# Performance work log

Hardware: AMD Instinct MI355X
Metric: run time of the kernel (lower is better)

The kernel has to match this reference:

```python
import jax, jax.numpy as jnp
import numpy as np

I, H, B, T = 17, 128, 32768, 19

def setup_inputs() -> dict:
    key = jax.random.key(0)
    ks = jax.random.split(key, 7)
    s = 1.0 / np.sqrt(H)  # PyTorch LSTMCell/Linear init scale
    u = lambda k, shape: jax.random.uniform(k, shape, jnp.float32, -s, s)
    return {
        "x": jax.random.normal(ks[0], (B, T, I), jnp.float32),
        "W_ih": u(ks[1], (4 * H, I)),
        "W_hh": u(ks[2], (4 * H, H)),
        "b_ih": u(ks[3], (4 * H,)),
        "b_hh": u(ks[4], (4 * H,)),
        "W_out": u(ks[5], (I, H)),
        "b_out": u(ks[6], (I,)),
    }

def reference(x, W_ih, W_hh, b_ih, b_hh, W_out, b_out):
    B_, T_, _ = x.shape
    Hh = W_hh.shape[1]
    # Precompute input projections for all timesteps in one GEMM: [B,T,4H]
    x_proj = jnp.einsum('bti,gi->btg', x, W_ih) + b_ih + b_hh

    def step(carry, xp_t):
        h, c = carry
        gates = xp_t + h @ W_hh.T            # [B,4H]
        i_g, f_g, g_g, o_g = jnp.split(gates, 4, axis=-1)
        c = jax.nn.sigmoid(f_g) * c + jax.nn.sigmoid(i_g) * jnp.tanh(g_g)
        h = jax.nn.sigmoid(o_g) * jnp.tanh(c)
        y = h @ W_out.T + b_out              # [B,I]
        return (h, c), y

    h0 = jnp.zeros((B_, Hh), x.dtype)
    c0 = jnp.zeros((B_, Hh), x.dtype)
    _, ys = jax.lax.scan(step, (h0, c0), jnp.swapaxes(x_proj, 0, 1))  # ys: [T,B,I]
    return jnp.swapaxes(ys, 0, 1)  # [B,T,I]
```

## Files before the change

kernel.cpp:

```cpp
#include <hip/hip_runtime.h>

#define I_DIM 17
#define H_DIM 128
#define T_DIM 19
#define B_DIM 32768
#define M_ROWS 128
#define NTHR 512
#define GRID (B_DIM / M_ROWS)
#define XI 323
#define NF (M_ROWS * XI)
#define XSLOT 4352

#define OFF_H 0
#define OFF_X 65536
#define OFF_WO 148224
#define LDS_TOT 156416

typedef __bf16 bf16x8 __attribute__((ext_vector_type(8)));
typedef float f32x4 __attribute__((ext_vector_type(4)));
union FragU { bf16x8 v; unsigned short s[8]; uint4 u; };

#define K1 1.4426950408889634f
#define K2 2.8853900817779268f

__device__ __forceinline__ unsigned short f2bf(float f) {
    union { float f; unsigned u; } x; x.f = f;
    return (unsigned short)((x.u + 0x8000u) >> 16);
}

#define SYNC_LDS() do {                                        \
    asm volatile("s_waitcnt lgkmcnt(0)" ::: "memory");         \
    __builtin_amdgcn_s_barrier();                              \
} while (0)

#define MFMA_Q(P_, QT_, ACC_, REC_) do {                                          \
    _Pragma("unroll") for (int m2 = 0; m2 < 2; ++m2) {                            \
        _Pragma("unroll") for (int g = 0; g < 4; ++g)                             \
            ACC_[m2][g] = (f32x4){bias[g], bias[g], bias[g], bias[g]};            \
        FragU fx; fx.u = (uint4){0u, 0u, 0u, 0u};                                 \
        if (q < 2)                                                                \
            fx.v = *(const bf16x8*)(smem + xyA + ((QT_) * 2 + m2) * 512);         \
        else if (q == 2)                                                          \
            fx.s[0] = *(const unsigned short*)(smem + xk16 + ((QT_) * 2 + m2) * 32); \
        _Pragma("unroll") for (int g = 0; g < 4; ++g)                             \
            ACC_[m2][g] = __builtin_amdgcn_mfma_f32_16x16x32_bf16(fx.v, wihr[g], ACC_[m2][g], 0, 0, 0); \
    }                                                                             \
    if (REC_) {                                                                   \
        _Pragma("unroll") for (int kk = 0; kk < 4; ++kk)                          \
            _Pragma("unroll") for (int m2 = 0; m2 < 2; ++m2) {                    \
                bf16x8 a = *(const bf16x8*)(smem + vkk[kk] + ((1 - (P_)) * 32768 + ((QT_) * 2 + m2) * 4096)); \
                _Pragma("unroll") for (int g = 0; g < 4; ++g)                     \
                    ACC_[m2][g] = __builtin_amdgcn_mfma_f32_16x16x32_bf16(a, whh[kk][g], ACC_[m2][g], 0, 0, 0); \
            }                                                                     \
    }                                                                             \
} while (0)

#define ELEM_Q(P_, QT_, ACC_) do {                                                \
    _Pragma("unroll") for (int m2 = 0; m2 < 2; ++m2)                              \
        _Pragma("unroll") for (int r = 0; r < 4; ++r) {                           \
            float ui = __builtin_amdgcn_exp2f(ACC_[m2][0][r]);                    \
            float uf = __builtin_amdgcn_exp2f(ACC_[m2][1][r]);                    \
            float vg = __builtin_amdgcn_exp2f(ACC_[m2][2][r]);                    \
            float uo = __builtin_amdgcn_exp2f(ACC_[m2][3][r]);                    \
            float A_ = 1.f + ui, F_ = 1.f + uf, G_ = 1.f + vg;                    \
            float AG = A_ * G_;                                                   \
            int ci = (QT_) * 8 + m2 * 4 + r;                                      \
            float c = (cst[ci] * AG + (1.f - vg) * F_) * __builtin_amdgcn_rcpf(F_ * AG); \
            cst[ci] = c;                                                          \
            float vc = __builtin_amdgcn_exp2f(-K2 * c);                           \
            float h = (1.f - vc) * __builtin_amdgcn_rcpf((1.f + uo) * (1.f + vc));\
            *(unsigned short*)(smem + vwr[r] + ((P_) * 32768 + ((QT_) * 2 + m2) * 4096)) = f2bf(h); \
        }                                                                         \
} while (0)

#define Y_BURST(P_) do {                                                          \
    f32x4 ya0 = {0.f, 0.f, 0.f, 0.f}, ya1 = {0.f, 0.f, 0.f, 0.f};                 \
    _Pragma("unroll") for (int kk = 0; kk < 4; ++kk) {                            \
        bf16x8 b  = *(const bf16x8*)(smem + vwo + kk * 1024);                     \
        bf16x8 a0 = *(const bf16x8*)(smem + vkk[kk] + vyk + (1 - (P_)) * 32768);  \
        bf16x8 a1 = *(const bf16x8*)(smem + vkk[kk] + vyk + (1 - (P_)) * 32768 + 16384); \
        ya0 = __builtin_amdgcn_mfma_f32_16x16x32_bf16(a0, b, ya0, 0, 0, 0);       \
        ya1 = __builtin_amdgcn_mfma_f32_16x16x32_bf16(a1, b, ya1, 0, 0, 0);       \
    }                                                                             \
    if (yok) {                                                                    \
        _Pragma("unroll") for (int r = 0; r < 4; ++r) {                           \
            ypt0[r * XI] = ya0[r] + ybo;                                          \
            ypt1[r * XI] = ya1[r] + ybo;                                          \
        }                                                                         \
    }                                                                             \
    ypt0 += I_DIM; ypt1 += I_DIM;                                                 \
} while (0)

#define STEP(P_) do {                      \
    MFMA_Q(P_, 0, accA, 1);                \
    MFMA_Q(P_, 1, accB, 1);                \
    ELEM_Q(P_, 0, accA);                   \
    MFMA_Q(P_, 2, accA, 1);                \
    ELEM_Q(P_, 1, accB);                   \
    MFMA_Q(P_, 3, accB, 1);                \
    ELEM_Q(P_, 2, accA);                   \
    Y_BURST(P_);                           \
    ELEM_Q(P_, 3, accB);                   \
    xyA += XSLOT; xk16 += XSLOT;           \
    SYNC_LDS();                            \
} while (0)

__global__ __launch_bounds__(NTHR)
__attribute__((amdgpu_waves_per_eu(2, 2)))
void flowlstm(
    const float* __restrict__ x, const float* __restrict__ W_ih,
    const float* __restrict__ W_hh, const float* __restrict__ b_ih,
    const float* __restrict__ b_hh, const float* __restrict__ W_out,
    const float* __restrict__ b_out, float* __restrict__ out)
{
    __shared__ __align__(16) unsigned char smem[LDS_TOT];
    const int tid = threadIdx.x;
    const int w = tid >> 6, lane = tid & 63, l15 = lane & 15, q = lane >> 4;
    const int cg = w;
    const int b0 = blockIdx.x * M_ROWS;

    {
        const float* xb = x + (size_t)b0 * XI;
        for (int j = 0; j < 81; ++j) {
            int f = tid + j * NTHR;
            if (f < NF) {
                float v = xb[f];
                unsigned uf_ = (unsigned)f;
                unsigned row = (uf_ * 51943u) >> 24;
                unsigned s = uf_ - row * 323u;
                unsigned t = (s * 61681u) >> 20;
                unsigned k = s - t * 17u;
                unsigned a;
                if (k == 16) a = OFF_X + t * XSLOT + 4096 + row * 2;
                else a = OFF_X + t * XSLOT + (row >> 4) * 512 + (k >> 3) * 256
                       + (row & 15) * 16 + (k & 7) * 2;
                *(unsigned short*)(smem + a) = f2bf(v);
            }
        }
    }
    {
        int ln = tid & 63, f = tid >> 6;
        int kk = f & 3, ct = f >> 2;
        int o = ct * 16 + (ln & 15);
        int kb = kk * 32 + (ln >> 4) * 8;
        FragU fu;
        #pragma unroll
        for (int e = 0; e < 8; ++e)
            fu.s[e] = (o < I_DIM) ? f2bf(W_out[o * H_DIM + kb + e]) : (unsigned short)0;
        *(uint4*)(smem + OFF_WO + f * 1024 + ln * 16) = fu.u;
    }
    float gsc[4] = { -K1, -K1, -K2, -K1 };

    bf16x8 whh[4][4];
    #pragma unroll
    for (int kk = 0; kk < 4; ++kk)
        #pragma unroll
        for (int g = 0; g < 4; ++g) {
            int n = g * H_DIM + cg * 16 + l15;
            const float* s = W_hh + n * H_DIM + kk * 32 + q * 8;
            FragU fu;
            #pragma unroll
            for (int e = 0; e < 8; ++e) fu.s[e] = f2bf(s[e] * gsc[g]);
            whh[kk][g] = fu.v;
        }
    bf16x8 wihr[4];
    #pragma unroll
    for (int g = 0; g < 4; ++g) {
        int n = g * H_DIM + cg * 16 + l15;
        FragU fu;
        #pragma unroll
        for (int e = 0; e < 8; ++e) {
            int k = q * 8 + e;
            fu.s[e] = (k < I_DIM) ? f2bf(W_ih[n * I_DIM + k] * gsc[g]) : (unsigned short)0;
        }
        wihr[g] = fu.v;
    }
    float bias[4];
    #pragma unroll
    for (int g = 0; g < 4; ++g) {
        int col = g * H_DIM + cg * 16 + l15;
        bias[g] = (b_ih[col] + b_hh[col]) * gsc[g];
    }
    const unsigned xr7 = (unsigned)((l15 & 7) << 4);
    unsigned vkk[4], vwr[4];
    #pragma unroll
    for (int kk = 0; kk < 4; ++kk)
        vkk[kk] = (unsigned)(l15 * 256 + ((kk * 64 + q * 16) ^ xr7));
    const int colh2 = (cg * 16 + l15) * 2;
    #pragma unroll
    for (int r = 0; r < 4; ++r) {
        int rq = q * 4 + r;
        vwr[r] = (unsigned)(rq * 256 + (colh2 ^ ((rq & 7) << 4)));
    }
    const int ymt = w >> 1, yct = w & 1;
    const int ycol = yct * 16 + l15;
    const unsigned vyk = (unsigned)(ymt * 4096);
    const unsigned vwo = (unsigned)(OFF_WO + yct * 4096 + lane * 16);
    const bool yok = (ycol < I_DIM);
    const float ybo = b_out[ycol < I_DIM ? ycol : 16];
    unsigned xyA  = (unsigned)(OFF_X + (q < 2 ? q * 256 : 0) + l15 * 16);
    unsigned xk16 = (unsigned)(OFF_X + 4096 + l15 * 2);
    float* ypt0 = out + (size_t)(b0 + ymt * 16 + q * 4) * XI + ycol;
    float* ypt1 = ypt0 + (size_t)64 * XI;

    float cst[32];
    #pragma unroll
    for (int i = 0; i < 32; ++i) cst[i] = 0.f;

    f32x4 accA[2][4], accB[2][4];

    __syncthreads();

    MFMA_Q(0, 0, accA, 0);
    MFMA_Q(0, 1, accB, 0);
    ELEM_Q(0, 0, accA);
    MFMA_Q(0, 2, accA, 0);
    ELEM_Q(0, 1, accB);
    MFMA_Q(0, 3, accB, 0);
    ELEM_Q(0, 2, accA);
    ELEM_Q(0, 3, accB);
    xyA += XSLOT; xk16 += XSLOT;
    SYNC_LDS();

    #pragma unroll 1
    for (int t = 1; t < T_DIM; t += 2) {
        STEP(1);
        STEP(0);
    }

    {
        f32x4 ya0 = {0.f, 0.f, 0.f, 0.f}, ya1 = {0.f, 0.f, 0.f, 0.f};
        #pragma unroll
        for (int kk = 0; kk < 4; ++kk) {
            bf16x8 b  = *(const bf16x8*)(smem + vwo + kk * 1024);
            bf16x8 a0 = *(const bf16x8*)(smem + vkk[kk] + vyk);
            bf16x8 a1 = *(const bf16x8*)(smem + vkk[kk] + vyk + 16384);
            ya0 = __builtin_amdgcn_mfma_f32_16x16x32_bf16(a0, b, ya0, 0, 0, 0);
            ya1 = __builtin_amdgcn_mfma_f32_16x16x32_bf16(a1, b, ya1, 0, 0, 0);
        }
        if (yok) {
            #pragma unroll
            for (int r = 0; r < 4; ++r) {
                ypt0[r * XI] = ya0[r] + ybo;
                ypt1[r * XI] = ya1[r] + ybo;
            }
        }
    }
}

extern "C" void kernel_launch(void* const* d_in, const int* in_sizes, int n_in,
                              void* d_out, int out_size, void* d_ws, size_t ws_size,
                              hipStream_t stream) {
    const float* x     = (const float*)d_in[0];
    const float* W_ih  = (const float*)d_in[1];
    const float* W_hh  = (const float*)d_in[2];
    const float* b_ih  = (const float*)d_in[3];
    const float* b_hh  = (const float*)d_in[4];
    const float* W_out = (const float*)d_in[5];
    const float* b_out = (const float*)d_in[6];
    float* out = (float*)d_out;

    dim3 grid(GRID), block(NTHR);
    flowlstm<<<grid, block, 0, stream>>>(x, W_ih, W_hh, b_ih, b_hh, W_out, b_out, out);
}
```

Before: 149.3 us.

## Transpose MFMA operands to pack h stores and vectorize output writes

Swaps the A/B operands of all MFMAs so each lane's accumulator holds four consecutive hidden columns of one row. This lets the bf16 h values be packed into a single 64-bit LDS store instead of four scalar stores, and lets output y be written as 16-byte float4 stores instead of strided scalars. Bias vectors become per-lane f32x4 and the Y-row mapping changes. It also adds sched_group_barrier hints interleaving MFMA, DS and VALU ops and replaces the manual waitcnt+barrier with __syncthreads, which could constrain the scheduler or add register pressure.

```diff
diff --git a/kernel.cpp b/kernel.cpp
--- a/kernel.cpp
+++ b/kernel.cpp
@@ -18,6 +18,7 @@
 
 typedef __bf16 bf16x8 __attribute__((ext_vector_type(8)));
 typedef float f32x4 __attribute__((ext_vector_type(4)));
+typedef float f32x4u __attribute__((ext_vector_type(4), aligned(4)));
 union FragU { bf16x8 v; unsigned short s[8]; uint4 u; };
 
 #define K1 1.4426950408889634f
@@ -28,35 +29,40 @@
     return (unsigned short)((x.u + 0x8000u) >> 16);
 }
 
-#define SYNC_LDS() do {                                        \
-    asm volatile("s_waitcnt lgkmcnt(0)" ::: "memory");         \
-    __builtin_amdgcn_s_barrier();                              \
+#define SGB_STEP() do {                                        \
+    _Pragma("unroll")                                          \
+    for (int it_ = 0; it_ < 32; ++it_) {                       \
+        __builtin_amdgcn_sched_group_barrier(0x100, 2, 0);     \
+        __builtin_amdgcn_sched_group_barrier(0x008, 5, 0);     \
+        __builtin_amdgcn_sched_group_barrier(0x002, 18, 0);    \
+    }                                                          \
 } while (0)
 
 #define MFMA_Q(P_, QT_, ACC_, REC_) do {                                          \
     _Pragma("unroll") for (int m2 = 0; m2 < 2; ++m2) {                            \
         _Pragma("unroll") for (int g = 0; g < 4; ++g)                             \
-            ACC_[m2][g] = (f32x4){bias[g], bias[g], bias[g], bias[g]};            \
+            ACC_[m2][g] = bias[g];                                                \
         FragU fx; fx.u = (uint4){0u, 0u, 0u, 0u};                                 \
         if (q < 2)                                                                \
             fx.v = *(const bf16x8*)(smem + xyA + ((QT_) * 2 + m2) * 512);         \
         else if (q == 2)                                                          \
             fx.s[0] = *(const unsigned short*)(smem + xk16 + ((QT_) * 2 + m2) * 32); \
         _Pragma("unroll") for (int g = 0; g < 4; ++g)                             \
-            ACC_[m2][g] = __builtin_amdgcn_mfma_f32_16x16x32_bf16(fx.v, wihr[g], ACC_[m2][g], 0, 0, 0); \
+            ACC_[m2][g] = __builtin_amdgcn_mfma_f32_16x16x32_bf16(wihr[g], fx.v, ACC_[m2][g], 0, 0, 0); \
     }                                                                             \
     if (REC_) {                                                                   \
         _Pragma("unroll") for (int kk = 0; kk < 4; ++kk)                          \
             _Pragma("unroll") for (int m2 = 0; m2 < 2; ++m2) {                    \
                 bf16x8 a = *(const bf16x8*)(smem + vkk[kk] + ((1 - (P_)) * 32768 + ((QT_) * 2 + m2) * 4096)); \
                 _Pragma("unroll") for (int g = 0; g < 4; ++g)                     \
-                    ACC_[m2][g] = __builtin_amdgcn_mfma_f32_16x16x32_bf16(a, whh[kk][g], ACC_[m2][g], 0, 0, 0); \
+                    ACC_[m2][g] = __builtin_amdgcn_mfma_f32_16x16x32_bf16(whh[kk][g], a, ACC_[m2][g], 0, 0, 0); \
             }                                                                     \
     }                                                                             \
 } while (0)
 
 #define ELEM_Q(P_, QT_, ACC_) do {                                                \
-    _Pragma("unroll") for (int m2 = 0; m2 < 2; ++m2)                              \
+    _Pragma("unroll") for (int m2 = 0; m2 < 2; ++m2) {                            \
+        unsigned long long hp = 0ull;                                             \
         _Pragma("unroll") for (int r = 0; r < 4; ++r) {                           \
             float ui = __builtin_amdgcn_exp2f(ACC_[m2][0][r]);                    \
             float uf = __builtin_amdgcn_exp2f(ACC_[m2][1][r]);                    \
@@ -69,24 +75,28 @@
             cst[ci] = c;                                                          \
             float vc = __builtin_amdgcn_exp2f(-K2 * c);                           \
             float h = (1.f - vc) * __builtin_amdgcn_rcpf((1.f + uo) * (1.f + vc));\
-            *(unsigned short*)(smem + vwr[r] + ((P_) * 32768 + ((QT_) * 2 + m2) * 4096)) = f2bf(h); \
+            union { float f; unsigned u; } hu; hu.f = h;                          \
+            hp |= (unsigned long long)((hu.u + 0x8000u) >> 16) << (16 * r);       \
         }                                                                         \
+        *(unsigned long long*)(smem + vwrT + ((P_) * 32768 + ((QT_) * 2 + m2) * 4096)) = hp; \
+    }                                                                             \
 } while (0)
 
 #define Y_BURST(P_) do {                                                          \
     f32x4 ya0 = {0.f, 0.f, 0.f, 0.f}, ya1 = {0.f, 0.f, 0.f, 0.f};                 \
     _Pragma("unroll") for (int kk = 0; kk < 4; ++kk) {                            \
-        bf16x8 b  = *(const bf16x8*)(smem + vwo + kk * 1024);                     \
-        bf16x8 a0 = *(const bf16x8*)(smem + vkk[kk] + vyk + (1 - (P_)) * 32768);  \
-        bf16x8 a1 = *(const bf16x8*)(smem + vkk[kk] + vyk + (1 - (P_)) * 32768 + 16384); \
-        ya0 = __builtin_amdgcn_mfma_f32_16x16x32_bf16(a0, b, ya0, 0, 0, 0);       \
-        ya1 = __builtin_amdgcn_mfma_f32_16x16x32_bf16(a1, b, ya1, 0, 0, 0);       \
-    }                                                                             \
-    if (yok) {                                                                    \
-        _Pragma("unroll") for (int r = 0; r < 4; ++r) {                           \
-            ypt0[r * XI] = ya0[r] + ybo;                                          \
-            ypt1[r * XI] = ya1[r] + ybo;                                          \
-        }                                                                         \
+        bf16x8 wa = *(const bf16x8*)(smem + vwo + kk * 1024);                     \
+        bf16x8 h0 = *(const bf16x8*)(smem + vkk[kk] + yrt + (1 - (P_)) * 32768);  \
+        bf16x8 h1 = *(const bf16x8*)(smem + vkk[kk] + yrt + 4096 + (1 - (P_)) * 32768); \
+        ya0 = __builtin_amdgcn_mfma_f32_16x16x32_bf16(wa, h0, ya0, 0, 0, 0);      \
+        ya1 = __builtin_amdgcn_mfma_f32_16x16x32_bf16(wa, h1, ya1, 0, 0, 0);      \
+    }                                                                             \
+    if (yct == 0) {                                                               \
+        *(f32x4u*)ypt0 = ya0 + ybo;                                               \
+        *(f32x4u*)ypt1 = ya1 + ybo;                                               \
+    } else if (q == 0) {                                                          \
+        ypt0[0] = ya0[0] + ybo[0];                                                \
+        ypt1[0] = ya1[0] + ybo[0];                                                \
     }                                                                             \
     ypt0 += I_DIM; ypt1 += I_DIM;                                                 \
 } while (0)
@@ -102,7 +112,8 @@
     Y_BURST(P_);                           \
     ELEM_Q(P_, 3, accB);                   \
     xyA += XSLOT; xk16 += XSLOT;           \
-    SYNC_LDS();                            \
+    SGB_STEP();                            \
+    __syncthreads();                       \
 } while (0)
 
 __global__ __launch_bounds__(NTHR)
@@ -175,33 +186,33 @@
         }
         wihr[g] = fu.v;
     }
-    float bias[4];
-    #pragma unroll
-    for (int g = 0; g < 4; ++g) {
-        int col = g * H_DIM + cg * 16 + l15;
-        bias[g] = (b_ih[col] + b_hh[col]) * gsc[g];
-    }
+    f32x4 bias[4];
+    #pragma unroll
+    for (int g = 0; g < 4; ++g)
+        #pragma unroll
+        for (int r = 0; r < 4; ++r) {
+            int col = g * H_DIM + cg * 16 + 4 * q + r;
+            bias[g][r] = (b_ih[col] + b_hh[col]) * gsc[g];
+        }
     const unsigned xr7 = (unsigned)((l15 & 7) << 4);
-    unsigned vkk[4], vwr[4];
+    unsigned vkk[4];
     #pragma unroll
     for (int kk = 0; kk < 4; ++kk)
         vkk[kk] = (unsigned)(l15 * 256 + ((kk * 64 + q * 16) ^ xr7));
-    const int colh2 = (cg * 16 + l15) * 2;
+    const unsigned vwrT = (unsigned)(l15 * 256 + (((cg * 16 + 4 * q) * 2) ^ xr7));
+    const int yct = w & 1;
+    const unsigned yrt = (unsigned)((w >> 1) * 8192);
+    const unsigned vwo = (unsigned)(OFF_WO + yct * 4096 + lane * 16);
+    f32x4 ybo;
     #pragma unroll
     for (int r = 0; r < 4; ++r) {
-        int rq = q * 4 + r;
-        vwr[r] = (unsigned)(rq * 256 + (colh2 ^ ((rq & 7) << 4)));
-    }
-    const int ymt = w >> 1, yct = w & 1;
-    const int ycol = yct * 16 + l15;
-    const unsigned vyk = (unsigned)(ymt * 4096);
-    const unsigned vwo = (unsigned)(OFF_WO + yct * 4096 + lane * 16);
-    const bool yok = (ycol < I_DIM);
-    const float ybo = b_out[ycol < I_DIM ? ycol : 16];
+        int col = yct * 16 + 4 * q + r;
+        ybo[r] = b_out[col < I_DIM ? col : 16];
+    }
     unsigned xyA  = (unsigned)(OFF_X + (q < 2 ? q * 256 : 0) + l15 * 16);
     unsigned xk16 = (unsigned)(OFF_X + 4096 + l15 * 2);
-    float* ypt0 = out + (size_t)(b0 + ymt * 16 + q * 4) * XI + ycol;
-    float* ypt1 = ypt0 + (size_t)64 * XI;
+    float* ypt0 = out + (size_t)(b0 + (w >> 1) * 32 + l15) * XI + (yct ? 16 : 4 * q);
+    float* ypt1 = ypt0 + (size_t)16 * XI;
 
     float cst[32];
     #pragma unroll
@@ -220,7 +231,7 @@
     ELEM_Q(0, 2, accA);
     ELEM_Q(0, 3, accB);
     xyA += XSLOT; xk16 += XSLOT;
-    SYNC_LDS();
+    __syncthreads();
 
     #pragma unroll 1
     for (int t = 1; t < T_DIM; t += 2) {
@@ -232,18 +243,18 @@
         f32x4 ya0 = {0.f, 0.f, 0.f, 0.f}, ya1 = {0.f, 0.f, 0.f, 0.f};
         #pragma unroll
         for (int kk = 0; kk < 4; ++kk) {
-            bf16x8 b  = *(const bf16x8*)(smem + vwo + kk * 1024);
-            bf16x8 a0 = *(const bf16x8*)(smem + vkk[kk] + vyk);
-            bf16x8 a1 = *(const bf16x8*)(smem + vkk[kk] + vyk + 16384);
-            ya0 = __builtin_amdgcn_mfma_f32_16x16x32_bf16(a0, b, ya0, 0, 0, 0);
-            ya1 = __builtin_amdgcn_mfma_f32_16x16x32_bf16(a1, b, ya1, 0, 0, 0);
-        }
-        if (yok) {
-            #pragma unroll
-            for (int r = 0; r < 4; ++r) {
-                ypt0[r * XI] = ya0[r] + ybo;
-                ypt1[r * XI] = ya1[r] + ybo;
-            }
+            bf16x8 wa = *(const bf16x8*)(smem + vwo + kk * 1024);
+            bf16x8 h0 = *(const bf16x8*)(smem + vkk[kk] + yrt);
+            bf16x8 h1 = *(const bf16x8*)(smem + vkk[kk] + yrt + 4096);
+            ya0 = __builtin_amdgcn_mfma_f32_16x16x32_bf16(wa, h0, ya0, 0, 0, 0);
+            ya1 = __builtin_amdgcn_mfma_f32_16x16x32_bf16(wa, h1, ya1, 0, 0, 0);
+        }
+        if (yct == 0) {
+            *(f32x4u*)ypt0 = ya0 + ybo;
+            *(f32x4u*)ypt1 = ya1 + ybo;
+        } else if (q == 0) {
+            ypt0[0] = ya0[0] + ybo[0];
+            ypt1[0] = ya1[0] + ybo[0];
         }
     }
 }
```

Result: no change. 150.0 us (+0.5%).
